# Kernel tuning notes

Measured on AMD Instinct MI355X. Metric: run time of the kernel, lower is better.

Reference implementation:

```python
import jax, jax.numpy as jnp
import numpy as np

B, L, H = 2, 2048, 2048
NH, NKV, HD = 16, 8, 128
K = 4            # conv kernel size
BASE = 1000000.0 # rotary base
H2 = NH // 2
N_REP = NH // NKV


def setup_inputs() -> dict:
    key = jax.random.key(0)
    ks = jax.random.split(key, 12)
    s = 0.02
    hidden_states = jax.random.normal(ks[0], (B, L, H), jnp.float32)
    idx = jnp.arange(L)
    diff = (idx[:, None] - idx[None, :]).astype(jnp.float32)
    # lightning-attention decay mask: -(i-j) on/below diagonal, -1e9 above
    lin_attention_mask = jnp.where(diff >= 0, -diff, -1e9).astype(jnp.float32)
    # additive causal mask for softmax half
    attention_mask = jnp.where(diff >= 0, 0.0, -1e9).astype(jnp.float32)[None, None]
    # ALiBi-style positive per-head slopes for the linear half
    slope_rate = (2.0 ** (-8.0 * jnp.arange(1, H2 + 1, dtype=jnp.float32) / H2)).reshape(H2, 1, 1)
    position_ids = jnp.arange(L, dtype=jnp.int32)
    Wq = s * jax.random.normal(ks[1], (H, H), jnp.float32)
    bq = jnp.zeros((H,), jnp.float32)
    Wk = s * jax.random.normal(ks[2], (H, NKV * HD), jnp.float32)
    bk = jnp.zeros((NKV * HD,), jnp.float32)
    Wv = s * jax.random.normal(ks[3], (H, NKV * HD), jnp.float32)
    bv = jnp.zeros((NKV * HD,), jnp.float32)
    Wo = s * jax.random.normal(ks[4], (H, H), jnp.float32)
    # conv init: identity tap at last index + tiny noise (matches _init_conv_to_one)
    q_conv_w = jnp.zeros((H // 2, K), jnp.float32).at[:, K - 1].set(1.0) + 1e-4 * jax.random.normal(ks[5], (H // 2, K), jnp.float32)
    q_conv_b = jnp.zeros((H // 2,), jnp.float32)
    k_conv_w = jnp.zeros((NKV * HD, K), jnp.float32).at[:, K - 1].set(1.0) + 1e-4 * jax.random.normal(ks[6], (NKV * HD, K), jnp.float32)
    k_conv_b = jnp.zeros((NKV * HD,), jnp.float32)
    return dict(hidden_states=hidden_states, lin_attention_mask=lin_attention_mask,
                attention_mask=attention_mask, slope_rate=slope_rate, position_ids=position_ids,
                Wq=Wq, bq=bq, Wk=Wk, bk=bk, Wv=Wv, bv=bv, Wo=Wo,
                q_conv_w=q_conv_w, q_conv_b=q_conv_b, k_conv_w=k_conv_w, k_conv_b=k_conv_b)


def _dwconv_causal(x, w, b):
    # x: [B,L,C]; w: [C,K]; b: [C]. Causal depthwise conv (torch Conv1d cross-correlation,
    # padding K-1 then truncate to first L positions).
    xp = jnp.pad(x, ((0, 0), (K - 1, 0), (0, 0)))
    y = b
    for i in range(K):
        y = y + xp[:, i:i + x.shape[1], :] * w[:, i]
    return y


def _rot_half(x):
    return jnp.concatenate([-x[..., HD // 2:], x[..., :HD // 2]], axis=-1)


def _rep_kv(x):
    # [B,NKV,L,D] -> [B,NH,L,D] via repeat_interleave on head dim
    return jnp.repeat(x, N_REP, axis=1)


def reference(hidden_states, lin_attention_mask, attention_mask, slope_rate, position_ids,
              Wq, bq, Wk, bk, Wv, bv, Wo, q_conv_w, q_conv_b, k_conv_w, k_conv_b):
    q = hidden_states @ Wq + bq          # [B,L,H]
    k = hidden_states @ Wk + bk          # [B,L,NKV*HD]
    v = hidden_states @ Wv + bv          # [B,L,NKV*HD]

    # ---- softmax half (first NH//2 heads, rotary) ----
    qs = q[..., :H // 2].reshape(B, L, H2, HD).transpose(0, 2, 1, 3)   # [B,H2,L,D]
    ks_ = k.reshape(B, L, NKV, HD).transpose(0, 2, 1, 3)               # [B,NKV,L,D]
    vs = v.reshape(B, L, NKV, HD).transpose(0, 2, 1, 3)
    inv_freq = 1.0 / (BASE ** (jnp.arange(0, HD, 2, dtype=jnp.float32) / HD))
    freqs = position_ids.astype(jnp.float32)[:, None] * inv_freq[None, :]
    emb = jnp.concatenate([freqs, freqs], axis=-1)                     # [L,D]
    cos, sin = jnp.cos(emb)[None, None], jnp.sin(emb)[None, None]
    qs = qs * cos + _rot_half(qs) * sin
    kr = ks_ * cos + _rot_half(ks_) * sin
    k_soft = _rep_kv(kr)[:, :H2]
    v_soft = _rep_kv(vs)[:, :H2]
    attn = jnp.einsum('bhnd,bhmd->bhnm', qs, k_soft) / np.sqrt(HD).astype(np.float32)
    attn = attn + attention_mask
    attn = jax.nn.softmax(attn.astype(jnp.float32), axis=-1).astype(qs.dtype)
    attn_out = jnp.einsum('bhnm,bhmd->bhnd', attn, v_soft)
    attn_out = attn_out.transpose(0, 2, 1, 3).reshape(B, L, H // 2)

    # ---- linear half (last NH//2 heads: conv -> silu -> decayed linear attention) ----
    q_tnorm = _dwconv_causal(q[..., H // 2:], q_conv_w, q_conv_b)      # [B,L,H/2]
    kc = _dwconv_causal(k, k_conv_w, k_conv_b)                          # [B,L,NKV*HD]
    qt = jax.nn.silu(q_tnorm).reshape(B, L, H2, HD).transpose(0, 2, 1, 3)
    kc = jax.nn.silu(kc).reshape(B, L, NKV, HD).transpose(0, 2, 1, 3)
    k_lin = _rep_kv(kc)[:, H2:]
    v_lin = _rep_kv(vs)[:, H2:]
    lin_mask = jnp.exp(slope_rate * lin_attention_mask)                 # [H2,L,L]
    energy = jnp.einsum('bhnd,bhmd->bhnm', qt, k_lin) * lin_mask
    out_t = jnp.einsum('bhnm,bhmd->bhnd', energy, v_lin)
    out_t = out_t.transpose(0, 2, 1, 3).reshape(B, L, H // 2)
    # SimpleRMSNorm (no weight), computed in fp32
    ot32 = out_t.astype(jnp.float32)
    out_t = (ot32 * jax.lax.rsqrt(jnp.mean(ot32 * ot32, axis=-1, keepdims=True) + 1e-6)).astype(out_t.dtype)

    return jnp.concatenate([attn_out, out_t], axis=-1) @ Wo
```

## Files before the change

kernel.cpp:

```cpp
#include <hip/hip_runtime.h>
#include <hip/hip_bf16.h>

typedef __attribute__((ext_vector_type(8))) short short8;
typedef __attribute__((ext_vector_type(4))) float f32x4;

__device__ __forceinline__ void gl_lds16(const void* g, void* l) {
    void* gp = const_cast<void*>(g);
    __builtin_amdgcn_global_load_lds((__attribute__((address_space(1))) void*)gp,
                                     (__attribute__((address_space(3))) void*)l, 16, 0, 0);
}
__device__ __forceinline__ short f2bf(float f) {
    __hip_bfloat16 h = __float2bfloat16(f);
    return __builtin_bit_cast(short, h);
}
__device__ __forceinline__ float bf2f(__hip_bfloat16 h) { return __bfloat162float(h); }
__device__ __forceinline__ float bfbits2f(short s) {
    unsigned int u = ((unsigned int)(unsigned short)s) << 16;
    return __builtin_bit_cast(float, u);
}
__device__ __forceinline__ void store_val(float* C, size_t i, float v) { C[i] = v; }
__device__ __forceinline__ void store_val(__hip_bfloat16* C, size_t i, float v) { C[i] = __float2bfloat16(v); }

__global__ __launch_bounds__(256) void cast_kernel(const float* __restrict__ in, __hip_bfloat16* __restrict__ out) {
    size_t i = (size_t)blockIdx.x * 256 + threadIdx.x;
    float4 v = ((const float4*)in)[i];
    ushort4 o;
    o.x = (unsigned short)f2bf(v.x); o.y = (unsigned short)f2bf(v.y);
    o.z = (unsigned short)f2bf(v.z); o.w = (unsigned short)f2bf(v.w);
    ((ushort4*)out)[i] = o;
}

__global__ __launch_bounds__(256) void biascat_kernel(const float* __restrict__ bq, const float* __restrict__ bk,
                                                      const float* __restrict__ bv, float* __restrict__ o) {
    int i = blockIdx.x * 256 + threadIdx.x;
    o[i] = (i < 2048) ? bq[i] : ((i < 3072) ? bk[i - 2048] : bv[i - 3072]);
}

__global__ __launch_bounds__(256) void transpose_w_kernel(const float* __restrict__ in, __hip_bfloat16* __restrict__ out, int R, int C) {
    __shared__ float tile[32][33];
    int c0 = blockIdx.x * 32, r0 = blockIdx.y * 32;
    int tx = threadIdx.x, ty = threadIdx.y;
#pragma unroll
    for (int i = 0; i < 4; ++i) tile[ty + i*8][tx] = in[(size_t)(r0 + ty + i*8) * C + c0 + tx];
    __syncthreads();
#pragma unroll
    for (int i = 0; i < 4; ++i) out[(size_t)(c0 + ty + i*8) * R + r0 + tx] = __float2bfloat16(tile[tx][ty + i*8]);
}

template <typename OutT, bool HAS_BIAS, bool SPLIT>
__global__ __launch_bounds__(256) void gemm_bt_kernel(
    const __hip_bfloat16* __restrict__ A, const __hip_bfloat16* __restrict__ Bt,
    const float* __restrict__ bias, OutT* __restrict__ C, OutT* __restrict__ C2,
    int M, int N, int K)
{
    __shared__ short As[128 * 64];
    __shared__ short Bs[128 * 64];
    int t = threadIdx.x, lane = t & 63, w = t >> 6;
    int m0 = blockIdx.y * 128, n0 = blockIdx.x * 128;
    int wr = (w >> 1) * 64, wc = (w & 1) * 64;
    f32x4 acc[4][4];
#pragma unroll
    for (int i = 0; i < 4; ++i)
#pragma unroll
        for (int j = 0; j < 4; ++j) acc[i][j] = (f32x4){0.f, 0.f, 0.f, 0.f};
    int srow = w * 8 + (lane >> 3);
    int scol = ((lane & 7) ^ (lane >> 3)) * 8;
    const __hip_bfloat16* Ag = A + (size_t)(m0 + srow) * K + scol;
    const __hip_bfloat16* Bg = Bt + (size_t)(n0 + srow) * K + scol;
    short* AsB = As + w * 8 * 64;
    short* BsB = Bs + w * 8 * 64;
    int c0l = lane & 15, quad = lane >> 4, sw8 = c0l & 7;
    for (int k0 = 0; k0 < K; k0 += 64) {
#pragma unroll
        for (int it = 0; it < 4; ++it) {
            gl_lds16(Ag + (size_t)it * 32 * K + k0, AsB + it * 32 * 64);
            gl_lds16(Bg + (size_t)it * 32 * K + k0, BsB + it * 32 * 64);
        }
        __syncthreads();
#pragma unroll
        for (int kk = 0; kk < 2; ++kk) {
            short8 a[4], b[4];
            int ch0 = (kk * 4 + quad) ^ sw8;
#pragma unroll
            for (int i = 0; i < 4; ++i)
                a[i] = *(const short8*)&As[(wr + i * 16 + c0l) * 64 + ch0 * 8];
#pragma unroll
            for (int i = 0; i < 4; ++i)
                b[i] = *(const short8*)&Bs[(wc + i * 16 + c0l) * 64 + ch0 * 8];
#pragma unroll
            for (int mi = 0; mi < 4; ++mi)
#pragma unroll
                for (int ni = 0; ni < 4; ++ni)
                    acc[mi][ni] = __builtin_amdgcn_mfma_f32_16x16x32_bf16(a[mi], b[ni], acc[mi][ni], 0, 0, 0);
        }
        __syncthreads();
    }
    bool hi = SPLIT && (n0 + wc) >= 2048;
    OutT* Cw = hi ? C2 : C;
    int nbase = SPLIT ? ((n0 + wc) - (hi ? 2048 : 0)) : (n0 + wc);
    int Nw = SPLIT ? 2048 : N;
#pragma unroll
    for (int ni = 0; ni < 4; ++ni) {
        int n = nbase + ni * 16 + c0l;
        float bias_v = HAS_BIAS ? bias[n0 + wc + ni * 16 + c0l] : 0.f;
#pragma unroll
        for (int mi = 0; mi < 4; ++mi) {
#pragma unroll
            for (int r = 0; r < 4; ++r) {
                int m = m0 + wr + mi * 16 + quad * 4 + r;
                store_val(Cw, (size_t)m * Nw + n, acc[mi][ni][r] + bias_v);
            }
        }
    }
}

__global__ __launch_bounds__(256) void ropeq_kernel(const __hip_bfloat16* __restrict__ qf, const int* __restrict__ pid, __hip_bfloat16* __restrict__ Qs) {
    size_t idx = (size_t)blockIdx.x * 256 + threadIdx.x;
    int c = idx & 1023; int l = (int)((idx >> 10) & 2047); int b = (int)(idx >> 21);
    int h = c >> 7, d = c & 127;
    int j = d & 63;
    float posv = (float)pid[l];
    float ang = posv * expf(-0.21586735246819178f * (float)j);
    float cs = cosf(ang), sn = sinf(ang);
    size_t row = (size_t)(b * 2048 + l) * 2048;
    float x = bf2f(qf[row + h * 128 + d]);
    float xr = (d < 64) ? -bf2f(qf[row + h * 128 + d + 64]) : bf2f(qf[row + h * 128 + d - 64]);
    Qs[(((size_t)(b * 8 + h) * 2048) + l) * 128 + d] = __float2bfloat16(x * cs + xr * sn);
}

__global__ __launch_bounds__(256) void ropek_kernel(const __hip_bfloat16* __restrict__ kvf, const int* __restrict__ pid, __hip_bfloat16* __restrict__ Ks) {
    size_t idx = (size_t)blockIdx.x * 256 + threadIdx.x;
    int cc = idx & 511; int l = (int)((idx >> 9) & 2047); int b = (int)(idx >> 20);
    int kvh = cc >> 7, d = cc & 127;
    int j = d & 63;
    float posv = (float)pid[l];
    float ang = posv * expf(-0.21586735246819178f * (float)j);
    float cs = cosf(ang), sn = sinf(ang);
    size_t row = (size_t)(b * 2048 + l) * 2048;
    float x = bf2f(kvf[row + kvh * 128 + d]);
    float xr = (d < 64) ? -bf2f(kvf[row + kvh * 128 + d + 64]) : bf2f(kvf[row + kvh * 128 + d - 64]);
    Ks[(((size_t)(b * 4 + kvh) * 2048) + l) * 128 + d] = __float2bfloat16(x * cs + xr * sn);
}

__global__ __launch_bounds__(256) void transpose_v_kernel(const __hip_bfloat16* __restrict__ kvf, __hip_bfloat16* __restrict__ Vt) {
    __shared__ __hip_bfloat16 tile[32][33];
    int l0 = blockIdx.x * 32, d0 = blockIdx.y * 32, bh = blockIdx.z;
    int b = bh >> 3, kvh = bh & 7;
    int tx = threadIdx.x, ty = threadIdx.y;
#pragma unroll
    for (int i = 0; i < 4; ++i)
        tile[ty + i*8][tx] = kvf[(size_t)(b * 2048 + l0 + ty + i*8) * 2048 + 1024 + kvh * 128 + d0 + tx];
    __syncthreads();
#pragma unroll
    for (int i = 0; i < 4; ++i)
        Vt[(size_t)(bh * 128 + d0 + ty + i*8) * 2048 + l0 + tx] = tile[tx][ty + i*8];
}

__global__ __launch_bounds__(256) void convq_kernel(const __hip_bfloat16* __restrict__ qf, const float* __restrict__ w, const float* __restrict__ bias, __hip_bfloat16* __restrict__ qt) {
    size_t idx = (size_t)blockIdx.x * 256 + threadIdx.x;
    int c = idx & 1023; int l = (int)((idx >> 10) & 2047); int b = (int)(idx >> 21);
    float y = bias[c];
#pragma unroll
    for (int i = 0; i < 4; ++i) {
        int ls = l - 3 + i;
        if (ls >= 0) y += w[c * 4 + i] * bf2f(qf[(size_t)(b * 2048 + ls) * 2048 + 1024 + c]);
    }
    y = y / (1.f + __expf(-y));
    qt[(((size_t)(b * 8 + (c >> 7)) * 2048) + l) * 128 + (c & 127)] = __float2bfloat16(y);
}

__global__ __launch_bounds__(256) void convk_kernel(const __hip_bfloat16* __restrict__ kvf, const float* __restrict__ w, const float* __restrict__ bias, __hip_bfloat16* __restrict__ kc) {
    size_t idx = (size_t)blockIdx.x * 256 + threadIdx.x;
    int cc = idx & 511; int l = (int)((idx >> 9) & 2047); int b = (int)(idx >> 20);
    int c = 512 + cc;
    float y = bias[c];
#pragma unroll
    for (int i = 0; i < 4; ++i) {
        int ls = l - 3 + i;
        if (ls >= 0) y += w[c * 4 + i] * bf2f(kvf[(size_t)(b * 2048 + ls) * 2048 + c]);
    }
    y = y / (1.f + __expf(-y));
    kc[(((size_t)(b * 4 + (cc >> 7)) * 2048) + l) * 128 + (cc & 127)] = __float2bfloat16(y);
}

__device__ __forceinline__ float redsum16(float v) {
    v += __shfl_xor(v, 1); v += __shfl_xor(v, 2);
    v += __shfl_xor(v, 4); v += __shfl_xor(v, 8);
    return v;
}
__device__ __forceinline__ void decode_slice(int x, int& q, int& jl, int& jh) {
    int sub;
    if (x < 8)       { q = x; sub = 0; }
    else if (x < 24) { q = 8 + ((x - 8) >> 1); sub = (x - 8) & 1; }
    else if (x < 48) { int u = x - 24; int d = u / 3; q = 16 + d; sub = u - 3 * d; }
    else             { int u = x - 48; q = 24 + (u >> 2); sub = u & 3; }
    jl = sub * 8;
    jh = min(jl + 8, q + 1);
}
__device__ __forceinline__ int slice_base(int q) {
    if (q < 8)  return q;
    if (q < 16) return 8 + 2 * (q - 8);
    if (q < 24) return 24 + 3 * (q - 16);
    return 48 + 4 * (q - 24);
}

__global__ __launch_bounds__(256, 4) void flash_part_kernel(
    const __hip_bfloat16* __restrict__ Qs, const __hip_bfloat16* __restrict__ Ks,
    const __hip_bfloat16* __restrict__ Vt, __hip_bfloat16* __restrict__ partO, float* __restrict__ partL)
{
    __shared__ short Kt[64 * 128];
    __shared__ short Vl[128 * 64];
    __shared__ short Pl[4][16 * 64];
    int x = blockIdx.x, bh = blockIdx.y;
    int q, jl, jh; decode_slice(x, q, jl, jh);
    int b = bh >> 3, h = bh & 7;
    int t = threadIdx.x, lane = t & 63, w = t >> 6, quad = lane >> 4, c0 = lane & 15;
    const __hip_bfloat16* Qrow = Qs + ((size_t)(b * 8 + h) * 2048 + q * 64 + w * 16 + c0) * 128;
    short8 qa[4];
#pragma unroll
    for (int kk = 0; kk < 4; ++kk) qa[kk] = *(const short8*)(Qrow + kk * 32 + quad * 8);
    const char* Kg = (const char*)(Ks + ((size_t)(b * 4 + (h >> 1)) * 2048) * 128);
    const __hip_bfloat16* Vg = Vt + (size_t)(b * 8 + (h >> 1)) * 128 * 2048;
    int rk = t >> 4, ck = (t & 15) ^ rk;
    int rv = t >> 3, cv = (t & 7) ^ (rv & 7);
    f32x4 O[8];
#pragma unroll
    for (int v = 0; v < 8; ++v) O[v] = (f32x4){0.f, 0.f, 0.f, 0.f};
    float lacc[4] = {0.f, 0.f, 0.f, 0.f};
    const float scale = 0.08838834764831845f;
    int gi0 = q * 64 + w * 16;
    for (int j0 = jl; j0 < jh; ++j0) {
#pragma unroll
        for (int it = 0; it < 4; ++it) {
            gl_lds16(Kg + (size_t)(j0 * 64 + it * 16 + rk) * 256 + ck * 16, (char*)Kt + it * 4096 + w * 1024);
            gl_lds16((const char*)(Vg + (size_t)(it * 32 + rv) * 2048 + j0 * 64 + cv * 8), (char*)Vl + it * 4096 + w * 1024);
        }
        __syncthreads();
        f32x4 S[4];
#pragma unroll
        for (int ni = 0; ni < 4; ++ni) S[ni] = (f32x4){0.f, 0.f, 0.f, 0.f};
#pragma unroll
        for (int kk = 0; kk < 4; ++kk) {
#pragma unroll
            for (int ni = 0; ni < 4; ++ni) {
                short8 bb = *(const short8*)&Kt[(ni * 16 + c0) * 128 + (((kk * 4 + quad) ^ c0) * 8)];
                S[ni] = __builtin_amdgcn_mfma_f32_16x16x32_bf16(qa[kk], bb, S[ni], 0, 0, 0);
            }
        }
        bool diag = (j0 == q);
#pragma unroll
        for (int ni = 0; ni < 4; ++ni) {
            int gj = j0 * 64 + ni * 16 + c0;
#pragma unroll
            for (int r = 0; r < 4; ++r) {
                int gi = gi0 + quad * 4 + r;
                float p = (diag && gj > gi) ? 0.f : __expf(S[ni][r] * scale);
                lacc[r] += p;
                int m = quad * 4 + r;
                Pl[w][m * 64 + (((ni * 2 + (c0 >> 3)) ^ (m & 7)) * 8) + (c0 & 7)] = f2bf(p);
            }
        }
#pragma unroll
        for (int kk = 0; kk < 2; ++kk) {
            short8 a = *(const short8*)&Pl[w][c0 * 64 + (((kk * 4 + quad) ^ (c0 & 7)) * 8)];
#pragma unroll
            for (int v = 0; v < 8; ++v) {
                short8 bb = *(const short8*)&Vl[(v * 16 + c0) * 64 + (((kk * 4 + quad) ^ (c0 & 7)) * 8)];
                O[v] = __builtin_amdgcn_mfma_f32_16x16x32_bf16(a, bb, O[v], 0, 0, 0);
            }
        }
        __syncthreads();
    }
#pragma unroll
    for (int r = 0; r < 4; ++r) {
        float lr = redsum16(lacc[r]);
        if (c0 == 0) partL[((size_t)(bh * 80 + x)) * 64 + w * 16 + quad * 4 + r] = lr;
    }
    size_t pb = (size_t)(bh * 80 + x) * 64 * 128;
#pragma unroll
    for (int v = 0; v < 8; ++v)
#pragma unroll
        for (int r = 0; r < 4; ++r)
            partO[pb + (size_t)(w * 16 + quad * 4 + r) * 128 + v * 16 + c0] = __float2bfloat16(O[v][r]);
}

__global__ __launch_bounds__(256) void flash_merge_kernel(const __hip_bfloat16* __restrict__ partO, const float* __restrict__ partL,
                                                          __hip_bfloat16* __restrict__ CC) {
    int q = blockIdx.x, bh = blockIdx.y, b = bh >> 3, h = bh & 7;
    int t = threadIdx.x, row = t >> 2, cg = (t & 3) * 32;
    int base = slice_base(q), ns = (q + 8) >> 3;
    float lt = 0.f;
    float acc[32];
#pragma unroll
    for (int i = 0; i < 32; ++i) acc[i] = 0.f;
    for (int s = 0; s < ns; ++s) {
        size_t sb = (size_t)(bh * 80 + base + s);
        lt += partL[sb * 64 + row];
        const short* po = (const short*)partO + (sb * 64 + row) * 128 + cg;
#pragma unroll
        for (int g = 0; g < 4; ++g) {
            short8 vv = *(const short8*)(po + g * 8);
#pragma unroll
            for (int e = 0; e < 8; ++e) acc[g * 8 + e] += bfbits2f(vv[e]);
        }
    }
    float inv = 1.f / lt;
    __hip_bfloat16* co = CC + ((size_t)(b * 2048 + q * 64 + row)) * 2048 + h * 128 + cg;
#pragma unroll
    for (int g = 0; g < 4; ++g) {
        short8 o;
#pragma unroll
        for (int e = 0; e < 8; ++e) o[e] = f2bf(acc[g * 8 + e] * inv);
        *(short8*)(co + g * 8) = o;
    }
}

__global__ __launch_bounds__(256, 4) void lin_part_kernel(
    const __hip_bfloat16* __restrict__ Qb, const __hip_bfloat16* __restrict__ Kb,
    const __hip_bfloat16* __restrict__ Vt, const float* __restrict__ slope, __hip_bfloat16* __restrict__ partO)
{
    __shared__ short Kt[64 * 128];
    __shared__ short Vl[128 * 64];
    __shared__ short Pl[4][16 * 64];
    int x = blockIdx.x, bh = blockIdx.y;
    int q, jl, jh; decode_slice(x, q, jl, jh);
    int b = bh >> 3, hh = bh & 7;
    float s = slope[hh];
    float thr = ((float)(q * 64) - 63.f - 25.f / s) * (1.f / 64.f);
    int jlo = thr > 0.f ? (int)ceilf(thr) : 0;
    if (jlo > q) jlo = q;
    int jstart = max(jl, jlo);
    if (jstart >= jh) return;
    int t = threadIdx.x, lane = t & 63, w = t >> 6, quad = lane >> 4, c0 = lane & 15;
    const __hip_bfloat16* Qrow = Qb + ((size_t)(b * 8 + hh) * 2048 + q * 64 + w * 16 + c0) * 128;
    short8 qa[4];
#pragma unroll
    for (int kk = 0; kk < 4; ++kk) qa[kk] = *(const short8*)(Qrow + kk * 32 + quad * 8);
    const char* Kg = (const char*)(Kb + ((size_t)(b * 4 + (hh >> 1)) * 2048) * 128);
    const __hip_bfloat16* Vg = Vt + (size_t)(b * 8 + 4 + (hh >> 1)) * 128 * 2048;
    int rk = t >> 4, ck = (t & 15) ^ rk;
    int rv = t >> 3, cv = (t & 7) ^ (rv & 7);
    f32x4 O[8];
#pragma unroll
    for (int v = 0; v < 8; ++v) O[v] = (f32x4){0.f, 0.f, 0.f, 0.f};
    int gi0 = q * 64 + w * 16;
    for (int j0 = jstart; j0 < jh; ++j0) {
#pragma unroll
        for (int it = 0; it < 4; ++it) {
            gl_lds16(Kg + (size_t)(j0 * 64 + it * 16 + rk) * 256 + ck * 16, (char*)Kt + it * 4096 + w * 1024);
            gl_lds16((const char*)(Vg + (size_t)(it * 32 + rv) * 2048 + j0 * 64 + cv * 8), (char*)Vl + it * 4096 + w * 1024);
        }
        __syncthreads();
        f32x4 S[4];
#pragma unroll
        for (int ni = 0; ni < 4; ++ni) S[ni] = (f32x4){0.f, 0.f, 0.f, 0.f};
#pragma unroll
        for (int kk = 0; kk < 4; ++kk) {
#pragma unroll
            for (int ni = 0; ni < 4; ++ni) {
                short8 bb = *(const short8*)&Kt[(ni * 16 + c0) * 128 + (((kk * 4 + quad) ^ c0) * 8)];
                S[ni] = __builtin_amdgcn_mfma_f32_16x16x32_bf16(qa[kk], bb, S[ni], 0, 0, 0);
            }
        }
        bool diag = (j0 == q);
#pragma unroll
        for (int ni = 0; ni < 4; ++ni) {
            int gj = j0 * 64 + ni * 16 + c0;
#pragma unroll
            for (int r = 0; r < 4; ++r) {
                int gi = gi0 + quad * 4 + r;
                float p = 0.f;
                if (!diag || gj <= gi) p = S[ni][r] * __expf(s * (float)(gj - gi));
                int m = quad * 4 + r;
                Pl[w][m * 64 + (((ni * 2 + (c0 >> 3)) ^ (m & 7)) * 8) + (c0 & 7)] = f2bf(p);
            }
        }
#pragma unroll
        for (int kk = 0; kk < 2; ++kk) {
            short8 a = *(const short8*)&Pl[w][c0 * 64 + (((kk * 4 + quad) ^ (c0 & 7)) * 8)];
#pragma unroll
            for (int v = 0; v < 8; ++v) {
                short8 bb = *(const short8*)&Vl[(v * 16 + c0) * 64 + (((kk * 4 + quad) ^ (c0 & 7)) * 8)];
                O[v] = __builtin_amdgcn_mfma_f32_16x16x32_bf16(a, bb, O[v], 0, 0, 0);
            }
        }
        __syncthreads();
    }
    size_t pb = (size_t)(bh * 80 + x) * 64 * 128;
#pragma unroll
    for (int v = 0; v < 8; ++v)
#pragma unroll
        for (int r = 0; r < 4; ++r)
            partO[pb + (size_t)(w * 16 + quad * 4 + r) * 128 + v * 16 + c0] = __float2bfloat16(O[v][r]);
}

__global__ __launch_bounds__(256) void lin_merge_kernel(const __hip_bfloat16* __restrict__ partO, const float* __restrict__ slope,
                                                        float* __restrict__ OT) {
    int q = blockIdx.x, bh = blockIdx.y, b = bh >> 3, hh = bh & 7;
    int t = threadIdx.x, row = t >> 2, cg = (t & 3) * 32;
    int base = slice_base(q), ns = (q + 8) >> 3;
    float s = slope[hh];
    float thr = ((float)(q * 64) - 63.f - 25.f / s) * (1.f / 64.f);
    int jlo = thr > 0.f ? (int)ceilf(thr) : 0;
    if (jlo > q) jlo = q;
    float acc[32];
#pragma unroll
    for (int i = 0; i < 32; ++i) acc[i] = 0.f;
    for (int s_ = 0; s_ < ns; ++s_) {
        int jl2 = s_ * 8, jh2 = min(jl2 + 8, q + 1);
        if (max(jl2, jlo) >= jh2) continue;
        size_t sb = (size_t)(bh * 80 + base + s_);
        const short* po = (const short*)partO + (sb * 64 + row) * 128 + cg;
#pragma unroll
        for (int g = 0; g < 4; ++g) {
            short8 vv = *(const short8*)(po + g * 8);
#pragma unroll
            for (int e = 0; e < 8; ++e) acc[g * 8 + e] += bfbits2f(vv[e]);
        }
    }
    float* oo = OT + ((size_t)(b * 2048 + q * 64 + row)) * 1024 + hh * 128 + cg;
#pragma unroll
    for (int g = 0; g < 8; ++g) {
        float4 o = make_float4(acc[g * 4], acc[g * 4 + 1], acc[g * 4 + 2], acc[g * 4 + 3]);
        ((float4*)oo)[g] = o;
    }
}

__global__ __launch_bounds__(256) void rmsnorm_kernel(const float* __restrict__ OT, __hip_bfloat16* __restrict__ CC) {
    int row = blockIdx.x;
    int t = threadIdx.x;
    float4 v = ((const float4*)(OT + (size_t)row * 1024))[t];
    float ss = v.x * v.x + v.y * v.y + v.z * v.z + v.w * v.w;
#pragma unroll
    for (int m = 1; m < 64; m <<= 1) ss += __shfl_xor(ss, m);
    __shared__ float red[4];
    if ((t & 63) == 0) red[t >> 6] = ss;
    __syncthreads();
    float tot = red[0] + red[1] + red[2] + red[3];
    float rs = rsqrtf(tot * (1.f / 1024.f) + 1e-6f);
    ushort4 o;
    o.x = (unsigned short)f2bf(v.x * rs); o.y = (unsigned short)f2bf(v.y * rs);
    o.z = (unsigned short)f2bf(v.z * rs); o.w = (unsigned short)f2bf(v.w * rs);
    *(ushort4*)(CC + (size_t)row * 2048 + 1024 + t * 4) = o;
}

extern "C" void kernel_launch(void* const* d_in, const int* in_sizes, int n_in,
                              void* d_out, int out_size, void* d_ws, size_t ws_size,
                              hipStream_t stream) {
    const float* hs   = (const float*)d_in[0];
    const float* slope= (const float*)d_in[3];
    const int*   pid  = (const int*)d_in[4];
    const float* Wq   = (const float*)d_in[5];
    const float* bq   = (const float*)d_in[6];
    const float* Wk   = (const float*)d_in[7];
    const float* bk   = (const float*)d_in[8];
    const float* Wv   = (const float*)d_in[9];
    const float* bv   = (const float*)d_in[10];
    const float* Wo   = (const float*)d_in[11];
    const float* qcw  = (const float*)d_in[12];
    const float* qcb  = (const float*)d_in[13];
    const float* kcw  = (const float*)d_in[14];
    const float* kcb  = (const float*)d_in[15];
    float* out = (float*)d_out;

    char* p = (char*)d_ws;
    auto alloc = [&](size_t bytes) { char* r = p; p += (bytes + 255) & ~(size_t)255; return r; };
    __hip_bfloat16* hsb   = (__hip_bfloat16*)alloc((size_t)4096 * 2048 * 2);
    __hip_bfloat16* bWqT  = (__hip_bfloat16*)alloc((size_t)2048 * 2048 * 2);
    __hip_bfloat16* bWkvT = (__hip_bfloat16*)alloc((size_t)2048 * 2048 * 2);
    __hip_bfloat16* bWoT  = (__hip_bfloat16*)alloc((size_t)2048 * 2048 * 2);
    float*          bqkv  = (float*)alloc(4096 * 4);
    __hip_bfloat16* qf    = (__hip_bfloat16*)alloc((size_t)4096 * 2048 * 2);
    __hip_bfloat16* kvf   = (__hip_bfloat16*)alloc((size_t)4096 * 2048 * 2);
    __hip_bfloat16* Qsb   = (__hip_bfloat16*)alloc((size_t)2 * 8 * 2048 * 128 * 2);
    __hip_bfloat16* Ksb   = (__hip_bfloat16*)alloc((size_t)2 * 4 * 2048 * 128 * 2);
    __hip_bfloat16* Vtb   = (__hip_bfloat16*)alloc((size_t)2 * 8 * 128 * 2048 * 2);
    __hip_bfloat16* qtb   = (__hip_bfloat16*)alloc((size_t)2 * 8 * 2048 * 128 * 2);
    __hip_bfloat16* kcbuf = (__hip_bfloat16*)alloc((size_t)2 * 4 * 2048 * 128 * 2);
    float*          OT    = (float*)alloc((size_t)2 * 2048 * 1024 * 4);
    __hip_bfloat16* CC    = (__hip_bfloat16*)alloc((size_t)4096 * 2048 * 2);

    __hip_bfloat16* partO = (__hip_bfloat16*)qf;
    float*          partL = (float*)((char*)kvf + (size_t)8 * 1024 * 1024);

    dim3 tb(32, 8);
    cast_kernel<<<8192, 256, 0, stream>>>(hs, hsb);
    biascat_kernel<<<16, 256, 0, stream>>>(bq, bk, bv, bqkv);
    transpose_w_kernel<<<dim3(64, 64), tb, 0, stream>>>(Wq, bWqT, 2048, 2048);
    transpose_w_kernel<<<dim3(32, 64), tb, 0, stream>>>(Wk, bWkvT, 2048, 1024);
    transpose_w_kernel<<<dim3(32, 64), tb, 0, stream>>>(Wv, bWkvT + (size_t)1024 * 2048, 2048, 1024);
    transpose_w_kernel<<<dim3(64, 64), tb, 0, stream>>>(Wo, bWoT, 2048, 2048);

    gemm_bt_kernel<__hip_bfloat16, true, true><<<dim3(32, 32), 256, 0, stream>>>(
        hsb, bWqT, bqkv, qf, kvf, 4096, 4096, 2048);

    ropeq_kernel<<<16384, 256, 0, stream>>>(qf, pid, Qsb);
    ropek_kernel<<<8192, 256, 0, stream>>>(kvf, pid, Ksb);
    transpose_v_kernel<<<dim3(64, 4, 16), tb, 0, stream>>>(kvf, Vtb);
    convq_kernel<<<16384, 256, 0, stream>>>(qf, qcw, qcb, qtb);
    convk_kernel<<<8192, 256, 0, stream>>>(kvf, kcw, kcb, kcbuf);

    flash_part_kernel<<<dim3(80, 16), 256, 0, stream>>>(Qsb, Ksb, Vtb, partO, partL);
    flash_merge_kernel<<<dim3(32, 16), 256, 0, stream>>>(partO, partL, CC);
    lin_part_kernel<<<dim3(80, 16), 256, 0, stream>>>(qtb, kcbuf, Vtb, slope, partO);
    lin_merge_kernel<<<dim3(32, 16), 256, 0, stream>>>(partO, slope, OT);
    rmsnorm_kernel<<<8192, 256, 0, stream>>>(OT, CC);

    gemm_bt_kernel<float, false, false><<<dim3(16, 32), 256, 0, stream>>>(
        CC, bWoT, nullptr, out, nullptr, 4096, 2048, 2048);
}
```

Before: 458.5 us.

## Use 32x32 MFMA in GEMMs and fuse prep, weight-transpose and merge/rmsnorm kernels

Switches the projection GEMMs from 16x16x32 to 32x32x16 bf16 MFMA tiles, which cuts the number of LDS fragment loads per MFMA. Merges the four weight-transpose launches into one vectorized 64x64-tile kernel. Fuses RoPE with the causal conv+SiLU for both Q and K. Folds the RMSNorm into the linear-attention merge so the fp32 OT round trip to memory goes away. The merge kernel now has far fewer blocks, each thread holding 64 accumulators, which may lower occupancy.

```diff
diff --git a/kernel.cpp b/kernel.cpp
--- a/kernel.cpp
+++ b/kernel.cpp
@@ -3,6 +3,7 @@
 
 typedef __attribute__((ext_vector_type(8))) short short8;
 typedef __attribute__((ext_vector_type(4))) float f32x4;
+typedef __attribute__((ext_vector_type(16))) float f32x16;
 
 __device__ __forceinline__ void gl_lds16(const void* g, void* l) {
     void* gp = const_cast<void*>(g);
@@ -36,15 +37,38 @@
     o[i] = (i < 2048) ? bq[i] : ((i < 3072) ? bk[i - 2048] : bv[i - 3072]);
 }
 
-__global__ __launch_bounds__(256) void transpose_w_kernel(const float* __restrict__ in, __hip_bfloat16* __restrict__ out, int R, int C) {
-    __shared__ float tile[32][33];
-    int c0 = blockIdx.x * 32, r0 = blockIdx.y * 32;
-    int tx = threadIdx.x, ty = threadIdx.y;
-#pragma unroll
-    for (int i = 0; i < 4; ++i) tile[ty + i*8][tx] = in[(size_t)(r0 + ty + i*8) * C + c0 + tx];
+__global__ __launch_bounds__(256) void transpose_w4_kernel(
+    const float* __restrict__ Wq, const float* __restrict__ Wo,
+    const float* __restrict__ Wk, const float* __restrict__ Wv,
+    __hip_bfloat16* __restrict__ oq, __hip_bfloat16* __restrict__ oo, __hip_bfloat16* __restrict__ okv)
+{
+    int z = blockIdx.z;
+    const float* in; __hip_bfloat16* out; int C;
+    if (z == 0)      { in = Wq; out = oq; C = 2048; }
+    else if (z == 1) { in = Wo; out = oo; C = 2048; }
+    else if (z == 2) { in = Wk; out = okv; C = 1024; }
+    else             { in = Wv; out = okv + (size_t)1024 * 2048; C = 1024; }
+    int c0 = blockIdx.x * 64, r0 = blockIdx.y * 64;
+    if (c0 >= C) return;
+    __shared__ float tile[64][65];
+    int t = threadIdx.x, tx = t & 15, ty = t >> 4;
+#pragma unroll
+    for (int i = 0; i < 4; ++i) {
+        float4 v = *(const float4*)(in + (size_t)(r0 + ty + i * 16) * C + c0 + tx * 4);
+        tile[ty + i * 16][tx * 4 + 0] = v.x; tile[ty + i * 16][tx * 4 + 1] = v.y;
+        tile[ty + i * 16][tx * 4 + 2] = v.z; tile[ty + i * 16][tx * 4 + 3] = v.w;
+    }
     __syncthreads();
 #pragma unroll
-    for (int i = 0; i < 4; ++i) out[(size_t)(c0 + ty + i*8) * R + r0 + tx] = __float2bfloat16(tile[tx][ty + i*8]);
+    for (int i = 0; i < 4; ++i) {
+        int lc = ty + i * 16, lr0 = tx * 4;
+        ushort4 o;
+        o.x = (unsigned short)f2bf(tile[lr0 + 0][lc]);
+        o.y = (unsigned short)f2bf(tile[lr0 + 1][lc]);
+        o.z = (unsigned short)f2bf(tile[lr0 + 2][lc]);
+        o.w = (unsigned short)f2bf(tile[lr0 + 3][lc]);
+        *(ushort4*)(out + (size_t)(c0 + lc) * 2048 + r0 + lr0) = o;
+    }
 }
 
 template <typename OutT, bool HAS_BIAS, bool SPLIT>
@@ -58,18 +82,20 @@
     int t = threadIdx.x, lane = t & 63, w = t >> 6;
     int m0 = blockIdx.y * 128, n0 = blockIdx.x * 128;
     int wr = (w >> 1) * 64, wc = (w & 1) * 64;
-    f32x4 acc[4][4];
-#pragma unroll
-    for (int i = 0; i < 4; ++i)
-#pragma unroll
-        for (int j = 0; j < 4; ++j) acc[i][j] = (f32x4){0.f, 0.f, 0.f, 0.f};
+    f32x16 acc[2][2];
+#pragma unroll
+    for (int i = 0; i < 2; ++i)
+#pragma unroll
+        for (int j = 0; j < 2; ++j)
+#pragma unroll
+            for (int e = 0; e < 16; ++e) acc[i][j][e] = 0.f;
     int srow = w * 8 + (lane >> 3);
     int scol = ((lane & 7) ^ (lane >> 3)) * 8;
     const __hip_bfloat16* Ag = A + (size_t)(m0 + srow) * K + scol;
     const __hip_bfloat16* Bg = Bt + (size_t)(n0 + srow) * K + scol;
     short* AsB = As + w * 8 * 64;
     short* BsB = Bs + w * 8 * 64;
-    int c0l = lane & 15, quad = lane >> 4, sw8 = c0l & 7;
+    int l31 = lane & 31, khalf = lane >> 5;
     for (int k0 = 0; k0 < K; k0 += 64) {
 #pragma unroll
         for (int it = 0; it < 4; ++it) {
@@ -78,20 +104,24 @@
         }
         __syncthreads();
 #pragma unroll
-        for (int kk = 0; kk < 2; ++kk) {
-            short8 a[4], b[4];
-            int ch0 = (kk * 4 + quad) ^ sw8;
-#pragma unroll
-            for (int i = 0; i < 4; ++i)
-                a[i] = *(const short8*)&As[(wr + i * 16 + c0l) * 64 + ch0 * 8];
-#pragma unroll
-            for (int i = 0; i < 4; ++i)
-                b[i] = *(const short8*)&Bs[(wc + i * 16 + c0l) * 64 + ch0 * 8];
-#pragma unroll
-            for (int mi = 0; mi < 4; ++mi)
-#pragma unroll
-                for (int ni = 0; ni < 4; ++ni)
-                    acc[mi][ni] = __builtin_amdgcn_mfma_f32_16x16x32_bf16(a[mi], b[ni], acc[mi][ni], 0, 0, 0);
+        for (int s = 0; s < 4; ++s) {
+            int chunk = s * 2 + khalf;
+            short8 a[2], b[2];
+#pragma unroll
+            for (int mi = 0; mi < 2; ++mi) {
+                int row = wr + mi * 32 + l31;
+                a[mi] = *(const short8*)&As[row * 64 + ((chunk ^ (row & 7)) * 8)];
+            }
+#pragma unroll
+            for (int ni = 0; ni < 2; ++ni) {
+                int row = wc + ni * 32 + l31;
+                b[ni] = *(const short8*)&Bs[row * 64 + ((chunk ^ (row & 7)) * 8)];
+            }
+#pragma unroll
+            for (int mi = 0; mi < 2; ++mi)
+#pragma unroll
+                for (int ni = 0; ni < 2; ++ni)
+                    acc[mi][ni] = __builtin_amdgcn_mfma_f32_32x32x16_bf16(a[mi], b[ni], acc[mi][ni], 0, 0, 0);
         }
         __syncthreads();
     }
@@ -100,46 +130,71 @@
     int nbase = SPLIT ? ((n0 + wc) - (hi ? 2048 : 0)) : (n0 + wc);
     int Nw = SPLIT ? 2048 : N;
 #pragma unroll
-    for (int ni = 0; ni < 4; ++ni) {
-        int n = nbase + ni * 16 + c0l;
-        float bias_v = HAS_BIAS ? bias[n0 + wc + ni * 16 + c0l] : 0.f;
-#pragma unroll
-        for (int mi = 0; mi < 4; ++mi) {
-#pragma unroll
-            for (int r = 0; r < 4; ++r) {
-                int m = m0 + wr + mi * 16 + quad * 4 + r;
-                store_val(Cw, (size_t)m * Nw + n, acc[mi][ni][r] + bias_v);
-            }
-        }
-    }
-}
-
-__global__ __launch_bounds__(256) void ropeq_kernel(const __hip_bfloat16* __restrict__ qf, const int* __restrict__ pid, __hip_bfloat16* __restrict__ Qs) {
+    for (int ni = 0; ni < 2; ++ni) {
+        float bias_v = HAS_BIAS ? bias[n0 + wc + ni * 32 + l31] : 0.f;
+        int n = nbase + ni * 32 + l31;
+#pragma unroll
+        for (int mi = 0; mi < 2; ++mi) {
+#pragma unroll
+            for (int reg = 0; reg < 16; ++reg) {
+                int m = m0 + wr + mi * 32 + (reg & 3) + 8 * (reg >> 2) + 4 * khalf;
+                store_val(Cw, (size_t)m * Nw + n, acc[mi][ni][reg] + bias_v);
+            }
+        }
+    }
+}
+
+__global__ __launch_bounds__(256) void prepq_kernel(const __hip_bfloat16* __restrict__ qf, const int* __restrict__ pid,
+                                                    const float* __restrict__ w, const float* __restrict__ bias,
+                                                    __hip_bfloat16* __restrict__ Qs, __hip_bfloat16* __restrict__ qt) {
     size_t idx = (size_t)blockIdx.x * 256 + threadIdx.x;
-    int c = idx & 1023; int l = (int)((idx >> 10) & 2047); int b = (int)(idx >> 21);
-    int h = c >> 7, d = c & 127;
-    int j = d & 63;
-    float posv = (float)pid[l];
-    float ang = posv * expf(-0.21586735246819178f * (float)j);
-    float cs = cosf(ang), sn = sinf(ang);
+    int c = idx & 2047; int l = (int)((idx >> 11) & 2047); int b = (int)(idx >> 22);
     size_t row = (size_t)(b * 2048 + l) * 2048;
-    float x = bf2f(qf[row + h * 128 + d]);
-    float xr = (d < 64) ? -bf2f(qf[row + h * 128 + d + 64]) : bf2f(qf[row + h * 128 + d - 64]);
-    Qs[(((size_t)(b * 8 + h) * 2048) + l) * 128 + d] = __float2bfloat16(x * cs + xr * sn);
-}
-
-__global__ __launch_bounds__(256) void ropek_kernel(const __hip_bfloat16* __restrict__ kvf, const int* __restrict__ pid, __hip_bfloat16* __restrict__ Ks) {
+    if (c < 1024) {
+        int h = c >> 7, d = c & 127, j = d & 63;
+        float posv = (float)pid[l];
+        float ang = posv * expf(-0.21586735246819178f * (float)j);
+        float cs = cosf(ang), sn = sinf(ang);
+        float x = bf2f(qf[row + c]);
+        float xr = (d < 64) ? -bf2f(qf[row + c + 64]) : bf2f(qf[row + c - 64]);
+        Qs[(((size_t)(b * 8 + h) * 2048) + l) * 128 + d] = __float2bfloat16(x * cs + xr * sn);
+    } else {
+        int ch = c - 1024;
+        float y = bias[ch];
+#pragma unroll
+        for (int i = 0; i < 4; ++i) {
+            int ls = l - 3 + i;
+            if (ls >= 0) y += w[ch * 4 + i] * bf2f(qf[(size_t)(b * 2048 + ls) * 2048 + 1024 + ch]);
+        }
+        y = y / (1.f + __expf(-y));
+        qt[(((size_t)(b * 8 + (ch >> 7)) * 2048) + l) * 128 + (ch & 127)] = __float2bfloat16(y);
+    }
+}
+
+__global__ __launch_bounds__(256) void prepk_kernel(const __hip_bfloat16* __restrict__ kvf, const int* __restrict__ pid,
+                                                    const float* __restrict__ w, const float* __restrict__ bias,
+                                                    __hip_bfloat16* __restrict__ Ks, __hip_bfloat16* __restrict__ kc) {
     size_t idx = (size_t)blockIdx.x * 256 + threadIdx.x;
-    int cc = idx & 511; int l = (int)((idx >> 9) & 2047); int b = (int)(idx >> 20);
-    int kvh = cc >> 7, d = cc & 127;
-    int j = d & 63;
-    float posv = (float)pid[l];
-    float ang = posv * expf(-0.21586735246819178f * (float)j);
-    float cs = cosf(ang), sn = sinf(ang);
+    int cc = idx & 1023; int l = (int)((idx >> 10) & 2047); int b = (int)(idx >> 21);
     size_t row = (size_t)(b * 2048 + l) * 2048;
-    float x = bf2f(kvf[row + kvh * 128 + d]);
-    float xr = (d < 64) ? -bf2f(kvf[row + kvh * 128 + d + 64]) : bf2f(kvf[row + kvh * 128 + d - 64]);
-    Ks[(((size_t)(b * 4 + kvh) * 2048) + l) * 128 + d] = __float2bfloat16(x * cs + xr * sn);
+    if (cc < 512) {
+        int kvh = cc >> 7, d = cc & 127, j = d & 63;
+        float posv = (float)pid[l];
+        float ang = posv * expf(-0.21586735246819178f * (float)j);
+        float cs = cosf(ang), sn = sinf(ang);
+        float x = bf2f(kvf[row + cc]);
+        float xr = (d < 64) ? -bf2f(kvf[row + cc + 64]) : bf2f(kvf[row + cc - 64]);
+        Ks[(((size_t)(b * 4 + kvh) * 2048) + l) * 128 + d] = __float2bfloat16(x * cs + xr * sn);
+    } else {
+        float y = bias[cc];
+#pragma unroll
+        for (int i = 0; i < 4; ++i) {
+            int ls = l - 3 + i;
+            if (ls >= 0) y += w[cc * 4 + i] * bf2f(kvf[(size_t)(b * 2048 + ls) * 2048 + cc]);
+        }
+        y = y / (1.f + __expf(-y));
+        kc[(((size_t)(b * 4 + ((cc - 512) >> 7)) * 2048) + l) * 128 + (cc & 127)] = __float2bfloat16(y);
+    }
 }
 
 __global__ __launch_bounds__(256) void transpose_v_kernel(const __hip_bfloat16* __restrict__ kvf, __hip_bfloat16* __restrict__ Vt) {
@@ -154,33 +209,6 @@
 #pragma unroll
     for (int i = 0; i < 4; ++i)
         Vt[(size_t)(bh * 128 + d0 + ty + i*8) * 2048 + l0 + tx] = tile[tx][ty + i*8];
-}
-
-__global__ __launch_bounds__(256) void convq_kernel(const __hip_bfloat16* __restrict__ qf, const float* __restrict__ w, const float* __restrict__ bias, __hip_bfloat16* __restrict__ qt) {
-    size_t idx = (size_t)blockIdx.x * 256 + threadIdx.x;
-    int c = idx & 1023; int l = (int)((idx >> 10) & 2047); int b = (int)(idx >> 21);
-    float y = bias[c];
-#pragma unroll
-    for (int i = 0; i < 4; ++i) {
-        int ls = l - 3 + i;
-        if (ls >= 0) y += w[c * 4 + i] * bf2f(qf[(size_t)(b * 2048 + ls) * 2048 + 1024 + c]);
-    }
-    y = y / (1.f + __expf(-y));
-    qt[(((size_t)(b * 8 + (c >> 7)) * 2048) + l) * 128 + (c & 127)] = __float2bfloat16(y);
-}
-
-__global__ __launch_bounds__(256) void convk_kernel(const __hip_bfloat16* __restrict__ kvf, const float* __restrict__ w, const float* __restrict__ bias, __hip_bfloat16* __restrict__ kc) {
-    size_t idx = (size_t)blockIdx.x * 256 + threadIdx.x;
-    int cc = idx & 511; int l = (int)((idx >> 9) & 2047); int b = (int)(idx >> 20);
-    int c = 512 + cc;
-    float y = bias[c];
-#pragma unroll
-    for (int i = 0; i < 4; ++i) {
-        int ls = l - 3 + i;
-        if (ls >= 0) y += w[c * 4 + i] * bf2f(kvf[(size_t)(b * 2048 + ls) * 2048 + c]);
-    }
-    y = y / (1.f + __expf(-y));
-    kc[(((size_t)(b * 4 + (cc >> 7)) * 2048) + l) * 128 + (cc & 127)] = __float2bfloat16(y);
 }
 
 __device__ __forceinline__ float redsum16(float v) {
@@ -394,54 +422,47 @@
             partO[pb + (size_t)(w * 16 + quad * 4 + r) * 128 + v * 16 + c0] = __float2bfloat16(O[v][r]);
 }
 
-__global__ __launch_bounds__(256) void lin_merge_kernel(const __hip_bfloat16* __restrict__ partO, const float* __restrict__ slope,
-                                                        float* __restrict__ OT) {
-    int q = blockIdx.x, bh = blockIdx.y, b = bh >> 3, hh = bh & 7;
-    int t = threadIdx.x, row = t >> 2, cg = (t & 3) * 32;
+__global__ __launch_bounds__(256) void lin_merge_rms_kernel(const __hip_bfloat16* __restrict__ partO, const float* __restrict__ slope,
+                                                            __hip_bfloat16* __restrict__ CC) {
+    int q = blockIdx.x, rg = blockIdx.y, b = blockIdx.z;
+    int t = threadIdx.x;
+    int row = rg * 16 + (t >> 4);
+    int seg = t & 15;
+    int hh = seg >> 1;
+    int cs = (seg & 1) * 64;
+    int bh = b * 8 + hh;
     int base = slice_base(q), ns = (q + 8) >> 3;
     float s = slope[hh];
     float thr = ((float)(q * 64) - 63.f - 25.f / s) * (1.f / 64.f);
     int jlo = thr > 0.f ? (int)ceilf(thr) : 0;
     if (jlo > q) jlo = q;
-    float acc[32];
-#pragma unroll
-    for (int i = 0; i < 32; ++i) acc[i] = 0.f;
+    float acc[64];
+#pragma unroll
+    for (int i = 0; i < 64; ++i) acc[i] = 0.f;
     for (int s_ = 0; s_ < ns; ++s_) {
         int jl2 = s_ * 8, jh2 = min(jl2 + 8, q + 1);
         if (max(jl2, jlo) >= jh2) continue;
-        size_t sb = (size_t)(bh * 80 + base + s_);
-        const short* po = (const short*)partO + (sb * 64 + row) * 128 + cg;
-#pragma unroll
-        for (int g = 0; g < 4; ++g) {
+        const short* po = (const short*)partO + ((size_t)(bh * 80 + base + s_) * 64 + row) * 128 + hh * 0 + cs;
+#pragma unroll
+        for (int g = 0; g < 8; ++g) {
             short8 vv = *(const short8*)(po + g * 8);
 #pragma unroll
             for (int e = 0; e < 8; ++e) acc[g * 8 + e] += bfbits2f(vv[e]);
         }
     }
-    float* oo = OT + ((size_t)(b * 2048 + q * 64 + row)) * 1024 + hh * 128 + cg;
+    float ss = 0.f;
+#pragma unroll
+    for (int i = 0; i < 64; ++i) ss += acc[i] * acc[i];
+    ss = redsum16(ss);
+    float rs = rsqrtf(ss * (1.f / 1024.f) + 1e-6f);
+    __hip_bfloat16* co = CC + ((size_t)(b * 2048 + q * 64 + row)) * 2048 + 1024 + hh * 128 + cs;
 #pragma unroll
     for (int g = 0; g < 8; ++g) {
-        float4 o = make_float4(acc[g * 4], acc[g * 4 + 1], acc[g * 4 + 2], acc[g * 4 + 3]);
-        ((float4*)oo)[g] = o;
-    }
-}
-
-__global__ __launch_bounds__(256) void rmsnorm_kernel(const float* __restrict__ OT, __hip_bfloat16* __restrict__ CC) {
-    int row = blockIdx.x;
-    int t = threadIdx.x;
-    float4 v = ((const float4*)(OT + (size_t)row * 1024))[t];
-    float ss = v.x * v.x + v.y * v.y + v.z * v.z + v.w * v.w;
-#pragma unroll
-    for (int m = 1; m < 64; m <<= 1) ss += __shfl_xor(ss, m);
-    __shared__ float red[4];
-    if ((t & 63) == 0) red[t >> 6] = ss;
-    __syncthreads();
-    float tot = red[0] + red[1] + red[2] + red[3];
-    float rs = rsqrtf(tot * (1.f / 1024.f) + 1e-6f);
-    ushort4 o;
-    o.x = (unsigned short)f2bf(v.x * rs); o.y = (unsigned short)f2bf(v.y * rs);
-    o.z = (unsigned short)f2bf(v.z * rs); o.w = (unsigned short)f2bf(v.w * rs);
-    *(ushort4*)(CC + (size_t)row * 2048 + 1024 + t * 4) = o;
+        short8 o;
+#pragma unroll
+        for (int e = 0; e < 8; ++e) o[e] = f2bf(acc[g * 8 + e] * rs);
+        *(short8*)(co + g * 8) = o;
+    }
 }
 
 extern "C" void kernel_launch(void* const* d_in, const int* in_sizes, int n_in,
@@ -477,34 +498,26 @@
     __hip_bfloat16* Vtb   = (__hip_bfloat16*)alloc((size_t)2 * 8 * 128 * 2048 * 2);
     __hip_bfloat16* qtb   = (__hip_bfloat16*)alloc((size_t)2 * 8 * 2048 * 128 * 2);
     __hip_bfloat16* kcbuf = (__hip_bfloat16*)alloc((size_t)2 * 4 * 2048 * 128 * 2);
-    float*          OT    = (float*)alloc((size_t)2 * 2048 * 1024 * 4);
     __hip_bfloat16* CC    = (__hip_bfloat16*)alloc((size_t)4096 * 2048 * 2);
 
     __hip_bfloat16* partO = (__hip_bfloat16*)qf;
     float*          partL = (float*)((char*)kvf + (size_t)8 * 1024 * 1024);
 
-    dim3 tb(32, 8);
     cast_kernel<<<8192, 256, 0, stream>>>(hs, hsb);
     biascat_kernel<<<16, 256, 0, stream>>>(bq, bk, bv, bqkv);
-    transpose_w_kernel<<<dim3(64, 64), tb, 0, stream>>>(Wq, bWqT, 2048, 2048);
-    transpose_w_kernel<<<dim3(32, 64), tb, 0, stream>>>(Wk, bWkvT, 2048, 1024);
-    transpose_w_kernel<<<dim3(32, 64), tb, 0, stream>>>(Wv, bWkvT + (size_t)1024 * 2048, 2048, 1024);
-    transpose_w_kernel<<<dim3(64, 64), tb, 0, stream>>>(Wo, bWoT, 2048, 2048);
+    transpose_w4_kernel<<<dim3(32, 32, 4), 256, 0, stream>>>(Wq, Wo, Wk, Wv, bWqT, bWoT, bWkvT);
 
     gemm_bt_kernel<__hip_bfloat16, true, true><<<dim3(32, 32), 256, 0, stream>>>(
         hsb, bWqT, bqkv, qf, kvf, 4096, 4096, 2048);
 
-    ropeq_kernel<<<16384, 256, 0, stream>>>(qf, pid, Qsb);
-    ropek_kernel<<<8192, 256, 0, stream>>>(kvf, pid, Ksb);
-    transpose_v_kernel<<<dim3(64, 4, 16), tb, 0, stream>>>(kvf, Vtb);
-    convq_kernel<<<16384, 256, 0, stream>>>(qf, qcw, qcb, qtb);
-    convk_kernel<<<8192, 256, 0, stream>>>(kvf, kcw, kcb, kcbuf);
+    prepq_kernel<<<32768, 256, 0, stream>>>(qf, pid, qcw, qcb, Qsb, qtb);
+    prepk_kernel<<<16384, 256, 0, stream>>>(kvf, pid, kcw, kcb, Ksb, kcbuf);
+    transpose_v_kernel<<<dim3(64, 4, 16), dim3(32, 8), 0, stream>>>(kvf, Vtb);
 
     flash_part_kernel<<<dim3(80, 16), 256, 0, stream>>>(Qsb, Ksb, Vtb, partO, partL);
     flash_merge_kernel<<<dim3(32, 16), 256, 0, stream>>>(partO, partL, CC);
     lin_part_kernel<<<dim3(80, 16), 256, 0, stream>>>(qtb, kcbuf, Vtb, slope, partO);
-    lin_merge_kernel<<<dim3(32, 16), 256, 0, stream>>>(partO, slope, OT);
-    rmsnorm_kernel<<<8192, 256, 0, stream>>>(OT, CC);
+    lin_merge_rms_kernel<<<dim3(32, 4, 2), 256, 0, stream>>>(partO, slope, CC);
 
     gemm_bt_kernel<float, false, false><<<dim3(16, 32), 256, 0, stream>>>(
         CC, bWoT, nullptr, out, nullptr, 4096, 2048, 2048);
```

After: 461.6 us. About the same (+0.7%).
